# Performance work log

Measured on AMD Instinct MI355X. Metric: run time of the kernel, lower is better.

## Reference

```python
import jax, jax.numpy as jnp
import numpy as np
from jax import lax

B, H_IN, W_IN = 2, 64, 64
C_FEAT = 256
HQ, WQ = 256, 256
HIDDEN_DEPTH = 4
IN_DIM = C_FEAT + 4  # q_feat + rel_coord(2) + rel_cell(2)
OUT_DIM = 2
EPS_SHIFT = 1e-6
CLAMP_EPS = 1e-6


def make_coord(h, w):
    # cell-center coords in [-1,1], dim 0 along H, dim 1 along W (LIIF convention)
    hs = (jnp.arange(h, dtype=jnp.float32) + 0.5) * (2.0 / h) - 1.0
    ws = (jnp.arange(w, dtype=jnp.float32) + 0.5) * (2.0 / w) - 1.0
    return jnp.stack(jnp.meshgrid(hs, ws, indexing='ij'), axis=-1)  # [h,w,2]


def setup_inputs() -> dict:
    key = jax.random.key(0)
    ks = jax.random.split(key, 16)
    inp = jax.random.normal(ks[0], (B, 3, H_IN, W_IN), dtype=jnp.float32)
    coord = jnp.broadcast_to(make_coord(HQ, WQ)[None], (B, HQ, WQ, 2)).astype(jnp.float32)
    cell = jnp.broadcast_to(jnp.array([2.0 / HQ, 2.0 / WQ], dtype=jnp.float32)[None], (B, 2))
    # encoder: single 3x3 conv 3 -> C_FEAT
    conv_w = jax.random.normal(ks[1], (C_FEAT, 3, 3, 3), dtype=jnp.float32) * (1.0 / np.sqrt(3 * 9))
    conv_b = jnp.zeros((C_FEAT,), dtype=jnp.float32)
    # imnet MLP: IN_DIM -> C_FEAT (xHIDDEN_DEPTH, ReLU) -> OUT_DIM
    w_in = jax.random.normal(ks[2], (IN_DIM, C_FEAT), dtype=jnp.float32) * (1.0 / np.sqrt(IN_DIM))
    b_in = jnp.zeros((C_FEAT,), dtype=jnp.float32)
    w_hid = jax.random.normal(ks[3], (HIDDEN_DEPTH - 1, C_FEAT, C_FEAT), dtype=jnp.float32) * (1.0 / np.sqrt(C_FEAT))
    b_hid = jnp.zeros((HIDDEN_DEPTH - 1, C_FEAT), dtype=jnp.float32)
    w_out = jax.random.normal(ks[4], (C_FEAT, OUT_DIM), dtype=jnp.float32) * (1.0 / np.sqrt(C_FEAT))
    b_out = jnp.zeros((OUT_DIM,), dtype=jnp.float32)
    return {"inp": inp, "coord": coord, "cell": cell, "conv_w": conv_w, "conv_b": conv_b,
            "w_in": w_in, "b_in": b_in, "w_hid": w_hid, "b_hid": b_hid,
            "w_out": w_out, "b_out": b_out}


def _mlp(x, w_in, b_in, w_hid, b_hid, w_out, b_out):
    h = jax.nn.relu(x @ w_in + b_in)
    for i in range(w_hid.shape[0]):
        h = jax.nn.relu(h @ w_hid[i] + b_hid[i])
    return h @ w_out + b_out


def _forward(inp, coord, cell, conv_w, conv_b, w_in, b_in, w_hid, b_hid, w_out, b_out):
    feat = lax.conv_general_dilated(inp, conv_w, (1, 1), 'SAME') + conv_b[None, :, None, None]
    Hf, Wf = feat.shape[-2], feat.shape[-1]
    rx = 1.0 / Hf  # 2/H/2
    ry = 1.0 / Wf
    gather = jax.vmap(lambda f, i, j: f[:, i, j])  # [C,H,W],[Hq,Wq]x2 -> [C,Hq,Wq]
    preds, areas = [], []
    for vx in (-1, 1):
        for vy in (-1, 1):
            ch = jnp.clip(coord[..., 0] + vx * rx + EPS_SHIFT, -1 + CLAMP_EPS, 1 - CLAMP_EPS)
            cw = jnp.clip(coord[..., 1] + vy * ry + EPS_SHIFT, -1 + CLAMP_EPS, 1 - CLAMP_EPS)
            # nearest-neighbor grid_sample (align_corners=False): idx = floor((g+1)*size/2)
            ih = jnp.clip(jnp.floor((ch + 1.0) * Hf * 0.5).astype(jnp.int32), 0, Hf - 1)
            iw = jnp.clip(jnp.floor((cw + 1.0) * Wf * 0.5).astype(jnp.int32), 0, Wf - 1)
            q_feat = gather(feat, ih, iw)  # [B,C,Hq,Wq]
            # sampled feat_coord equals cell-center coord of the nearest pixel
            q_ch = (2.0 * ih.astype(jnp.float32) + 1.0) / Hf - 1.0
            q_cw = (2.0 * iw.astype(jnp.float32) + 1.0) / Wf - 1.0
            rel_h = (coord[..., 0] - q_ch) * Hf  # [B,Hq,Wq]
            rel_w = (coord[..., 1] - q_cw) * Wf
            rc_h = jnp.broadcast_to((cell[:, 0] * Hf)[:, None, None], rel_h.shape)
            rc_w = jnp.broadcast_to((cell[:, 1] * Wf)[:, None, None], rel_w.shape)
            x = jnp.concatenate([
                jnp.moveaxis(q_feat, 1, -1),  # [B,Hq,Wq,C]
                rel_h[..., None], rel_w[..., None], rc_h[..., None], rc_w[..., None]
            ], axis=-1)
            preds.append(_mlp(x, w_in, b_in, w_hid, b_hid, w_out, b_out))  # [B,Hq,Wq,2]
            areas.append(jnp.abs(rel_h * rel_w) + 1e-9)
    tot_area = areas[0] + areas[1] + areas[2] + areas[3]
    # local-ensemble diagonal swap
    areas[0], areas[3] = areas[3], areas[0]
    areas[1], areas[2] = areas[2], areas[1]
    ret = sum(p * (a / tot_area)[..., None] for p, a in zip(preds, areas))
    ret = jax.nn.softmax(ret, axis=-1)
    return jnp.moveaxis(ret, -1, 1)  # [B,2,Hq,Wq]


def reference(inp, coord, cell, conv_w, conv_b, w_in, b_in, w_hid, b_hid, w_out, b_out):
    return _forward(inp, coord, cell, conv_w, conv_b, w_in, b_in, w_hid, b_hid, w_out, b_out)
```

## Files before the change

### kernel.cpp

```cpp
#include <hip/hip_runtime.h>

typedef unsigned short ushort_t;
typedef __attribute__((ext_vector_type(8))) _Float16 f16x8;
typedef __attribute__((ext_vector_type(4))) float f32x4;
typedef __attribute__((ext_vector_type(4))) unsigned int u32x4;
typedef __attribute__((ext_vector_type(2))) unsigned long long u64x2;

#define ROWB 576
#define BUFB (64*ROWB)

__device__ __forceinline__ ushort_t f2h(float x){ _Float16 h=(_Float16)x; return __builtin_bit_cast(ushort_t,h); }
__device__ __forceinline__ float h2f(ushort_t u){ return (float)__builtin_bit_cast(_Float16,u); }
__device__ __forceinline__ unsigned int pkrtz(float lo, float hi){
    return __builtin_bit_cast(unsigned int, __builtin_amdgcn_cvt_pkrtz(lo, hi));
}
__device__ __forceinline__ unsigned int pk_add2(unsigned int a, unsigned int b){
    unsigned int r; asm("v_pk_add_f16 %0, %1, %2" : "=v"(r) : "v"(a), "v"(b)); return r;
}
__device__ __forceinline__ unsigned int pk_relu2(unsigned int a){
    unsigned int r; asm("v_pk_max_f16 %0, %1, %2" : "=v"(r) : "v"(a), "v"(0u)); return r;
}

__device__ __forceinline__ int permc(int c){
    return (c & ~31) + (((c >> 2) & 3) << 3) + (c & 3) + (((c >> 4) & 1) << 2);
}

__global__ __launch_bounds__(256) void conv_k(const float* __restrict__ inp,
        const float* __restrict__ w, const float* __restrict__ bias,
        ushort_t* __restrict__ feat)
{
    __shared__ float sw_[6912];
    __shared__ float patch[27];
    int t = threadIdx.x;
    int b = blockIdx.x >> 12, p = blockIdx.x & 4095;
    int y = p >> 6, x = p & 63;
    for (int i = t; i < 6912; i += 256) sw_[i] = w[i];
    if (t < 27){
        int ci = t/9, r = t%9, dy = r/3, dx = r%3;
        int yy = y+dy-1, xx = x+dx-1;
        patch[t] = (yy>=0 && yy<64 && xx>=0 && xx<64) ? inp[((b*3+ci)<<12)+(yy<<6)+xx] : 0.f;
    }
    __syncthreads();
    float acc = bias[t];
    #pragma unroll
    for (int j = 0; j < 27; ++j) acc += patch[j]*sw_[t*27+j];
    feat[(((b<<12)+p)<<8) + permc(t)] = f2h(acc);
}

__global__ __launch_bounds__(256) void pack_k(const float* __restrict__ w_in,
        const float* __restrict__ w_hid, ushort_t* __restrict__ packW)
{
    int i = blockIdx.x*256 + threadIdx.x;
    if (i >= 270336) return;
    int layer, rem;
    if (i < 73728){ layer = 0; rem = i; }
    else { int j = i - 73728; layer = 1 + (j >> 16); rem = j & 65535; }
    int j8 = rem & 7, frag = rem >> 3;
    int lane = frag & 63, kt = frag >> 6;
    int kc = kt >> 4, nt = kt & 15;
    int k = kc*32 + ((lane>>4)<<2) + (j8 & 3) + ((j8 >> 2) << 4);
    int n = (nt<<4) + (lane & 15);
    float val;
    if (layer == 0) val = (k < 260) ? w_in[k*256 + n] : 0.f;
    else            val = w_hid[((layer-1)*256 + k)*256 + n];
    packW[i] = f2h(val);
}

__global__ __launch_bounds__(256) void l0pre_k(const ushort_t* feat,
        const ushort_t* __restrict__ packW, ushort_t* h0)
{
    __shared__ __align__(16) char buf[BUFB];
    const int t = threadIdx.x, lane = t & 63, wave = t >> 6;
    const int b = blockIdx.x >> 6, p0 = (blockIdx.x & 63) << 6;
    {
        int m = t >> 2, q = t & 3;
        char* drow = buf + m*ROWB;
        int sw = ((m & 7) << 4) ^ (q << 4);
        const u64x2* src = (const u64x2*)(feat + (((b<<12) + p0 + m)<<8) + q*64);
        #pragma unroll
        for (int c = 0; c < 8; ++c)
            *(u64x2*)(drow + ((q*128 + c*16) ^ sw)) = src[c];
    }
    __syncthreads();
    const int l15 = lane & 15, g = lane >> 4;
    const int swz = (l15 & 7) << 4;
    f32x4 acc[4][4];
    #pragma unroll
    for (int nt = 0; nt < 4; ++nt)
        #pragma unroll
        for (int mg = 0; mg < 4; ++mg) acc[mg][nt] = (f32x4){0.f,0.f,0.f,0.f};
    const int lofs = (wave*256 + lane)*8;
    f16x8 wA[4], wB[4], aP0[4], aP1[4];
    #pragma unroll
    for (int nt = 0; nt < 4; ++nt){
        wA[nt] = *(const f16x8*)(packW + lofs + nt*512);
        wB[nt] = *(const f16x8*)(packW + lofs + 8192 + nt*512);
    }
    {
        const int o2 = (g*16) ^ swz;
        #pragma unroll
        for (int mg = 0; mg < 4; ++mg)
            aP0[mg] = *(const f16x8*)(buf + (mg*16 + l15)*ROWB + o2);
    }
    #pragma unroll
    for (int kc = 0; kc < 8; ++kc){
        if (kc + 1 < 8){
            const int o2 = ((kc + 1)*64 + g*16) ^ swz ^ ((((kc + 1) >> 1) & 3) << 4);
            if ((kc & 1) == 0){
                #pragma unroll
                for (int mg = 0; mg < 4; ++mg)
                    aP1[mg] = *(const f16x8*)(buf + (mg*16 + l15)*ROWB + o2);
            } else {
                #pragma unroll
                for (int mg = 0; mg < 4; ++mg)
                    aP0[mg] = *(const f16x8*)(buf + (mg*16 + l15)*ROWB + o2);
            }
        }
        if ((kc & 1) == 0){
            #pragma unroll
            for (int mg = 0; mg < 4; ++mg)
                #pragma unroll
                for (int nt = 0; nt < 4; ++nt)
                    acc[mg][nt] = __builtin_amdgcn_mfma_f32_16x16x32_f16(wA[nt], aP0[mg], acc[mg][nt], 0, 0, 0);
        } else {
            #pragma unroll
            for (int mg = 0; mg < 4; ++mg)
                #pragma unroll
                for (int nt = 0; nt < 4; ++nt)
                    acc[mg][nt] = __builtin_amdgcn_mfma_f32_16x16x32_f16(wB[nt], aP1[mg], acc[mg][nt], 0, 0, 0);
        }
        if (kc + 2 < 8){
            const ushort_t* pf = packW + lofs + (kc + 2)*8192;
            if ((kc & 1) == 0){
                #pragma unroll
                for (int nt = 0; nt < 4; ++nt) wA[nt] = *(const f16x8*)(pf + nt*512);
            } else {
                #pragma unroll
                for (int nt = 0; nt < 4; ++nt) wB[nt] = *(const f16x8*)(pf + nt*512);
            }
        }
    }
    #pragma unroll
    for (int mg = 0; mg < 4; ++mg){
        char* row = (char*)(h0 + (((b<<12) + p0 + mg*16 + l15)<<8));
        #pragma unroll
        for (int i = 0; i < 2; ++i){
            const int kb = 2*wave + i;
            f32x4 a0 = acc[mg][2*i], a1 = acc[mg][2*i + 1];
            u32x4 st;
            st[0] = pkrtz(a0[0], a0[1]);
            st[1] = pkrtz(a0[2], a0[3]);
            st[2] = pkrtz(a1[0], a1[1]);
            st[3] = pkrtz(a1[2], a1[3]);
            *(u32x4*)(row + kb*64 + 16*g) = st;
        }
    }
}

template<int KC, bool HAS_NEXT, bool STORE>
__device__ __forceinline__ void mlp_layer(const ushort_t* __restrict__ wfrag,
        const ushort_t* __restrict__ nextw,
        const float* __restrict__ bias, char* __restrict__ buf,
        int lane, int wave, f16x8 (&wP0)[4], f16x8 (&wP1)[4], f32x4 (&acc)[4][4])
{
    const int l15 = lane & 15, g = lane >> 4;
    const int swz  = (l15 & 7) << 4;
    const int aoffg = g*16;
    #pragma unroll
    for (int nt = 0; nt < 4; ++nt){
        f32x4 bv = *(const f32x4*)(bias + (wave*4 + nt)*16 + 4*g);
        #pragma unroll
        for (int mg = 0; mg < 4; ++mg) acc[mg][nt] = bv;
    }
    const int lofs = (wave*4*64 + lane)*8;
    f16x8 aP0[4], aP1[4];
    {
        const int o2 = aoffg ^ swz;
        #pragma unroll
        for (int mg = 0; mg < 4; ++mg)
            aP0[mg] = *(const f16x8*)(buf + (mg*16 + l15)*ROWB + o2);
    }
    #pragma unroll
    for (int kc = 0; kc < KC; ++kc){
        const ushort_t* pfw = nullptr;
        if (kc + 2 < KC)   pfw = wfrag + lofs + (kc + 2)*8192;
        else if (HAS_NEXT) pfw = nextw + lofs + (kc + 2 - KC)*8192;
        const bool la = (kc + 1 < KC);
        if (la){
            const int o2 = ((kc + 1)*64 + aoffg) ^ swz ^ ((((kc + 1) >> 1) & 3) << 4);
            if ((kc & 1) == 0){
                #pragma unroll
                for (int mg = 0; mg < 4; ++mg)
                    aP1[mg] = *(const f16x8*)(buf + (mg*16 + l15)*ROWB + o2);
            } else {
                #pragma unroll
                for (int mg = 0; mg < 4; ++mg)
                    aP0[mg] = *(const f16x8*)(buf + (mg*16 + l15)*ROWB + o2);
            }
        }
        __builtin_amdgcn_s_setprio(1);
        if ((kc & 1) == 0){
            #pragma unroll
            for (int mg = 0; mg < 4; ++mg)
                #pragma unroll
                for (int nt = 0; nt < 4; ++nt)
                    acc[mg][nt] = __builtin_amdgcn_mfma_f32_16x16x32_f16(wP0[nt], aP0[mg], acc[mg][nt], 0, 0, 0);
        } else {
            #pragma unroll
            for (int mg = 0; mg < 4; ++mg)
                #pragma unroll
                for (int nt = 0; nt < 4; ++nt)
                    acc[mg][nt] = __builtin_amdgcn_mfma_f32_16x16x32_f16(wP1[nt], aP1[mg], acc[mg][nt], 0, 0, 0);
        }
        __builtin_amdgcn_s_setprio(0);
        if (pfw){
            if ((kc & 1) == 0){
                #pragma unroll
                for (int nt = 0; nt < 4; ++nt) wP0[nt] = *(const f16x8*)(pfw + nt*512);
            } else {
                #pragma unroll
                for (int nt = 0; nt < 4; ++nt) wP1[nt] = *(const f16x8*)(pfw + nt*512);
            }
        }
    }
    __syncthreads();
    if (STORE){
        const int wsw = swz ^ (wave << 4);
        #pragma unroll
        for (int mg = 0; mg < 4; ++mg){
            char* row = buf + (mg*16 + l15)*ROWB;
            #pragma unroll
            for (int i = 0; i < 2; ++i){
                const int kb = 2*wave + i;
                f32x4 a0 = acc[mg][2*i], a1 = acc[mg][2*i + 1];
                u32x4 st;
                st[0] = pk_relu2(pkrtz(a0[0], a0[1]));
                st[1] = pk_relu2(pkrtz(a0[2], a0[3]));
                st[2] = pk_relu2(pkrtz(a1[0], a1[1]));
                st[3] = pk_relu2(pkrtz(a1[2], a1[3]));
                *(u32x4*)(row + ((kb*64 + 16*g) ^ wsw)) = st;
            }
        }
        __syncthreads();
    }
}

__global__ __launch_bounds__(256, 3) void liif_k(
        const float* __restrict__ coord, const float* __restrict__ cell,
        const float* __restrict__ b_in, const float* __restrict__ b_hid,
        const float* __restrict__ w_out, const float* __restrict__ b_out,
        const ushort_t* __restrict__ h0, const ushort_t* __restrict__ packW,
        float* __restrict__ out)
{
    __shared__ __align__(16) char buf[BUFB];
    __shared__ float sarea[64];
    const int t = threadIdx.x, lane = t & 63, wave = t >> 6;
    const int bi = blockIdx.x;
    const int b = bi >> 12;
    const int t12 = bi & 4095;
    const int th = t12 >> 6, tw = t12 & 63;

    f16x8 wX[4], wA[4], wB[4];
    const ushort_t* L1 = packW + 73728;
    {
        const int lofs = (wave*256 + lane)*8;
        #pragma unroll
        for (int nt = 0; nt < 4; ++nt){
            wX[nt] = *(const f16x8*)(packW + 65536 + lofs + nt*512);
            wA[nt] = *(const f16x8*)(L1 + lofs + nt*512);
            wB[nt] = *(const f16x8*)(L1 + 8192 + nt*512 + lofs);
        }
    }

    {
        int m = t >> 2, q = t & 3;
        int v = m >> 4, pix = m & 15;
        int qh = th*4 + (pix >> 2), qw = tw*4 + (pix & 3);
        int cidx = (((b<<8) + qh)<<8) + qw;
        float c0 = coord[cidx*2], c1 = coord[cidx*2 + 1];
        float ch = c0 + ((v & 2) ? 0.015625f : -0.015625f); ch = ch + 1e-6f;
        ch = fminf(fmaxf(ch, -1.f + 1e-6f), 1.f - 1e-6f);
        float cw = c1 + ((v & 1) ? 0.015625f : -0.015625f); cw = cw + 1e-6f;
        cw = fminf(fmaxf(cw, -1.f + 1e-6f), 1.f - 1e-6f);
        int ih = (int)floorf((ch + 1.f)*64.f*0.5f); ih = ih < 0 ? 0 : (ih > 63 ? 63 : ih);
        int iw = (int)floorf((cw + 1.f)*64.f*0.5f); iw = iw < 0 ? 0 : (iw > 63 ? 63 : iw);
        char* drow = buf + m*ROWB;
        int sw = ((m & 7) << 4) ^ (q << 4);
        const u64x2* src = (const u64x2*)(h0 + ((((b<<6) + ih)<<6) + iw)*256 + q*64);
        #pragma unroll
        for (int c = 0; c < 8; ++c)
            *(u64x2*)(drow + ((q*128 + c*16) ^ sw)) = src[c];
        if (q == 0){
            float qch = (2.f*(float)ih + 1.f)*(1.f/64.f) - 1.f;
            float qcw = (2.f*(float)iw + 1.f)*(1.f/64.f) - 1.f;
            float relh = (c0 - qch)*64.f, relw = (c1 - qcw)*64.f;
            float rch = cell[b*2]*64.f, rcw = cell[b*2 + 1]*64.f;
            unsigned long long ex = (unsigned long long)f2h(relh)
                | ((unsigned long long)f2h(relw) << 16)
                | ((unsigned long long)f2h(rch)  << 32)
                | ((unsigned long long)f2h(rcw)  << 48);
            u64x2 e; e[0] = ex; e[1] = 0;
            u64x2 z; z[0] = 0;  z[1] = 0;
            int sw2 = (m & 3) << 4;
            #pragma unroll
            for (int c = 1; c < 4; ++c)
                *(u64x2*)(drow + 512 + ((c*16) ^ sw2)) = z;
            *(u64x2*)(drow + 512 + sw2) = e;
            sarea[m] = fabsf(relh*relw) + 1e-9f;
        }
    }
    __syncthreads();

    f32x4 acc[4][4];
    {
        const int l15 = lane & 15, g = lane >> 4;
        const int swz  = (l15 & 7) << 4;
        const int swz2 = (l15 & 3) << 4;
        const int wsw  = swz ^ (wave << 4);
        #pragma unroll
        for (int nt = 0; nt < 4; ++nt){
            f32x4 bv = *(const f32x4*)(b_in + (wave*4 + nt)*16 + 4*g);
            #pragma unroll
            for (int mg = 0; mg < 4; ++mg) acc[mg][nt] = bv;
        }
        f16x8 af[4];
        {
            const int o2 = 512 + ((g*16) ^ swz2);
            #pragma unroll
            for (int mg = 0; mg < 4; ++mg)
                af[mg] = *(const f16x8*)(buf + (mg*16 + l15)*ROWB + o2);
        }
        #pragma unroll
        for (int mg = 0; mg < 4; ++mg)
            #pragma unroll
            for (int nt = 0; nt < 4; ++nt)
                acc[mg][nt] = __builtin_amdgcn_mfma_f32_16x16x32_f16(wX[nt], af[mg], acc[mg][nt], 0, 0, 0);
        #pragma unroll
        for (int mg = 0; mg < 4; ++mg){
            char* row = buf + (mg*16 + l15)*ROWB;
            #pragma unroll
            for (int i = 0; i < 2; ++i){
                const int kb = 2*wave + i;
                u32x4 hv = *(const u32x4*)(row + ((kb*64 + 16*g) ^ wsw));
                f32x4 a0 = acc[mg][2*i], a1 = acc[mg][2*i + 1];
                u32x4 st;
                st[0] = pk_relu2(pk_add2(pkrtz(a0[0], a0[1]), hv[0]));
                st[1] = pk_relu2(pk_add2(pkrtz(a0[2], a0[3]), hv[1]));
                st[2] = pk_relu2(pk_add2(pkrtz(a1[0], a1[1]), hv[2]));
                st[3] = pk_relu2(pk_add2(pkrtz(a1[2], a1[3]), hv[3]));
                *(u32x4*)(row + ((kb*64 + 16*g) ^ wsw)) = st;
            }
        }
        __syncthreads();
    }

    const ushort_t* L2 = packW + 73728 + 65536;
    const ushort_t* L3 = packW + 73728 + 131072;
    mlp_layer<8, true , true >(L1, L2,      b_hid,       buf, lane, wave, wA, wB, acc);
    mlp_layer<8, true , true >(L2, L3,      b_hid + 256, buf, lane, wave, wA, wB, acc);
    mlp_layer<8, false, false>(L3, nullptr, b_hid + 512, buf, lane, wave, wA, wB, acc);

    {
        const int l15 = lane & 15, g = lane >> 4;
        float s0[4] = {0.f,0.f,0.f,0.f}, s1[4] = {0.f,0.f,0.f,0.f};
        #pragma unroll
        for (int j = 0; j < 4; ++j){
            int nb = wave*64 + j*16 + 4*g;
            f32x4 w01 = *(const f32x4*)(w_out + nb*2);
            f32x4 w23 = *(const f32x4*)(w_out + nb*2 + 4);
            #pragma unroll
            for (int mg = 0; mg < 4; ++mg){
                float v0 = fmaxf(acc[mg][j][0], 0.f);
                float v1 = fmaxf(acc[mg][j][1], 0.f);
                float v2 = fmaxf(acc[mg][j][2], 0.f);
                float v3 = fmaxf(acc[mg][j][3], 0.f);
                s0[mg] += v0*w01[0] + v1*w01[2] + v2*w23[0] + v3*w23[2];
                s1[mg] += v0*w01[1] + v1*w01[3] + v2*w23[1] + v3*w23[3];
            }
        }
        float2* stage  = (float2*)buf;
        float2* stage2 = (float2*)(buf + 2048);
        #pragma unroll
        for (int mg = 0; mg < 4; ++mg){
            s0[mg] += __shfl_xor(s0[mg], 16); s0[mg] += __shfl_xor(s0[mg], 32);
            s1[mg] += __shfl_xor(s1[mg], 16); s1[mg] += __shfl_xor(s1[mg], 32);
            if (lane < 16){
                float2 pr; pr.x = s0[mg]; pr.y = s1[mg];
                stage[wave*64 + mg*16 + l15] = pr;
            }
        }
        __syncthreads();
        if (t < 64){
            float2 p0 = stage[t], p1 = stage[64 + t], p2 = stage[128 + t], p3 = stage[192 + t];
            float2 pr;
            pr.x = p0.x + p1.x + p2.x + p3.x;
            pr.y = p0.y + p1.y + p2.y + p3.y;
            stage2[t] = pr;
        }
        __syncthreads();
        if (t < 16){
            float2 pv[4]; float a[4];
            #pragma unroll
            for (int v = 0; v < 4; ++v){
                pv[v] = stage2[v*16 + t];
                a[v]  = sarea[v*16 + t];
            }
            float tot = a[0] + a[1] + a[2] + a[3];
            float w0 = a[3]/tot, w1 = a[2]/tot, w2 = a[1]/tot, w3 = a[0]/tot;
            float r0 = pv[0].x*w0 + pv[1].x*w1 + pv[2].x*w2 + pv[3].x*w3 + b_out[0];
            float r1 = pv[0].y*w0 + pv[1].y*w1 + pv[2].y*w2 + pv[3].y*w3 + b_out[1];
            float mx = fmaxf(r0, r1);
            float e0 = expf(r0 - mx), e1 = expf(r1 - mx);
            float inv = 1.f/(e0 + e1);
            int qh = th*4 + (t >> 2), qw = tw*4 + (t & 3);
            int qidx = (qh << 8) + qw;
            out[(b<<17) + qidx]         = e0*inv;
            out[(b<<17) + 65536 + qidx] = e1*inv;
        }
    }
}

extern "C" void kernel_launch(void* const* d_in, const int* in_sizes, int n_in,
                              void* d_out, int out_size, void* d_ws, size_t ws_size,
                              hipStream_t stream)
{
    const float* inp   = (const float*)d_in[0];
    const float* coord = (const float*)d_in[1];
    const float* cell  = (const float*)d_in[2];
    const float* convw = (const float*)d_in[3];
    const float* convb = (const float*)d_in[4];
    const float* w_in  = (const float*)d_in[5];
    const float* b_in  = (const float*)d_in[6];
    const float* w_hid = (const float*)d_in[7];
    const float* b_hid = (const float*)d_in[8];
    const float* w_out = (const float*)d_in[9];
    const float* b_out = (const float*)d_in[10];
    (void)in_sizes; (void)n_in; (void)out_size; (void)ws_size;

    char* ws = (char*)d_ws;
    ushort_t* feat  = (ushort_t*)ws;
    ushort_t* packW = (ushort_t*)(ws + 4194304);
    float* out = (float*)d_out;

    pack_k<<<dim3(1056), dim3(256), 0, stream>>>(w_in, w_hid, packW);
    conv_k<<<dim3(8192), dim3(256), 0, stream>>>(inp, convw, convb, feat);
    l0pre_k<<<dim3(128), dim3(256), 0, stream>>>(feat, packW, feat);
    liif_k<<<dim3(8192), dim3(256), 0, stream>>>(coord, cell, b_in, b_hid,
                                                 w_out, b_out, feat, packW, out);
}
```

Measured before the change: 258.1 us.

## Fuse 3x3 conv into layer-0 pre-GEMM kernel using MFMA on 8x8 spatial tiles

Removes the separate per-pixel scalar conv kernel, which ran 8192 blocks each reloading the full conv weights. The conv is now computed inside the layer-0 projection kernel as a K=32 MFMA over im2col patches built in LDS from 8x8 spatial tiles. The fp16 result goes back into LDS, so the full feature map no longer makes a round trip through global memory. Conv weights are packed to fp16 fragments alongside the MLP weights. This adds fp16 rounding of conv inputs and weights, and rows of h0 are now written in tile order.

```diff
diff --git a/kernel.cpp b/kernel.cpp
--- a/kernel.cpp
+++ b/kernel.cpp
@@ -25,33 +25,21 @@
     return (c & ~31) + (((c >> 2) & 3) << 3) + (c & 3) + (((c >> 4) & 1) << 2);
 }
 
-__global__ __launch_bounds__(256) void conv_k(const float* __restrict__ inp,
-        const float* __restrict__ w, const float* __restrict__ bias,
-        ushort_t* __restrict__ feat)
-{
-    __shared__ float sw_[6912];
-    __shared__ float patch[27];
-    int t = threadIdx.x;
-    int b = blockIdx.x >> 12, p = blockIdx.x & 4095;
-    int y = p >> 6, x = p & 63;
-    for (int i = t; i < 6912; i += 256) sw_[i] = w[i];
-    if (t < 27){
-        int ci = t/9, r = t%9, dy = r/3, dx = r%3;
-        int yy = y+dy-1, xx = x+dx-1;
-        patch[t] = (yy>=0 && yy<64 && xx>=0 && xx<64) ? inp[((b*3+ci)<<12)+(yy<<6)+xx] : 0.f;
-    }
-    __syncthreads();
-    float acc = bias[t];
-    #pragma unroll
-    for (int j = 0; j < 27; ++j) acc += patch[j]*sw_[t*27+j];
-    feat[(((b<<12)+p)<<8) + permc(t)] = f2h(acc);
-}
-
 __global__ __launch_bounds__(256) void pack_k(const float* __restrict__ w_in,
-        const float* __restrict__ w_hid, ushort_t* __restrict__ packW)
+        const float* __restrict__ w_hid, const float* __restrict__ convw,
+        ushort_t* __restrict__ packW)
 {
     int i = blockIdx.x*256 + threadIdx.x;
-    if (i >= 270336) return;
+    if (i >= 278528) return;
+    if (i >= 270336){
+        int j = i - 270336;
+        int j8 = j & 7, frag = j >> 3;
+        int lane = frag & 63, nt = frag >> 6;
+        int k = ((lane>>4)<<2) + (j8 & 3) + ((j8 >> 2) << 4);
+        int n = (nt<<4) + (lane & 15);
+        packW[i] = f2h(k < 27 ? convw[n*27 + k] : 0.f);
+        return;
+    }
     int layer, rem;
     if (i < 73728){ layer = 0; rem = i; }
     else { int j = i - 73728; layer = 1 + (j >> 16); rem = j & 65535; }
@@ -66,83 +54,156 @@
     packW[i] = f2h(val);
 }
 
-__global__ __launch_bounds__(256) void l0pre_k(const ushort_t* feat,
-        const ushort_t* __restrict__ packW, ushort_t* h0)
+__global__ __launch_bounds__(256) void convl0_k(const float* __restrict__ inp,
+        const float* __restrict__ convb, const ushort_t* __restrict__ packW,
+        ushort_t* __restrict__ h0)
 {
     __shared__ __align__(16) char buf[BUFB];
+    __shared__ float patch[300];
     const int t = threadIdx.x, lane = t & 63, wave = t >> 6;
-    const int b = blockIdx.x >> 6, p0 = (blockIdx.x & 63) << 6;
+    const int b = blockIdx.x >> 6, tile = blockIdx.x & 63;
+    const int ty = tile >> 3, tx = tile & 7;
+
+    for (int i = t; i < 300; i += 256){
+        int ci = i / 100, rem = i % 100, py = rem / 10, px = rem % 10;
+        int gy = ty*8 + py - 1, gx = tx*8 + px - 1;
+        patch[i] = (gy >= 0 && gy < 64 && gx >= 0 && gx < 64)
+                 ? inp[((b*3 + ci) << 12) + (gy << 6) + gx] : 0.f;
+    }
+    __syncthreads();
+
     {
         int m = t >> 2, q = t & 3;
-        char* drow = buf + m*ROWB;
-        int sw = ((m & 7) << 4) ^ (q << 4);
-        const u64x2* src = (const u64x2*)(feat + (((b<<12) + p0 + m)<<8) + q*64);
-        #pragma unroll
-        for (int c = 0; c < 8; ++c)
-            *(u64x2*)(drow + ((q*128 + c*16) ^ sw)) = src[c];
+        int my = m >> 3, mx = m & 7;
+        ushort_t vals[8];
+        #pragma unroll
+        for (int j = 0; j < 8; ++j){
+            int k = 4*q + (j & 3) + ((j >> 2) << 4);
+            float v = 0.f;
+            if (k < 27){
+                int ci = k / 9, r = k % 9;
+                v = patch[ci*100 + (my + r/3)*10 + (mx + r%3)];
+            }
+            vals[j] = f2h(v);
+        }
+        u64x2 st;
+        st[0] = (unsigned long long)vals[0] | ((unsigned long long)vals[1] << 16)
+              | ((unsigned long long)vals[2] << 32) | ((unsigned long long)vals[3] << 48);
+        st[1] = (unsigned long long)vals[4] | ((unsigned long long)vals[5] << 16)
+              | ((unsigned long long)vals[6] << 32) | ((unsigned long long)vals[7] << 48);
+        *(u64x2*)(buf + m*ROWB + ((q*16) ^ ((m & 7) << 4))) = st;
     }
     __syncthreads();
+
     const int l15 = lane & 15, g = lane >> 4;
     const int swz = (l15 & 7) << 4;
     f32x4 acc[4][4];
+
+    #pragma unroll
+    for (int nt = 0; nt < 4; ++nt){
+        f32x4 bv = *(const f32x4*)(convb + (wave*4 + nt)*16 + 4*g);
+        #pragma unroll
+        for (int mg = 0; mg < 4; ++mg) acc[mg][nt] = bv;
+    }
+    {
+        const ushort_t* packC = packW + 270336;
+        const int lofs = (wave*4*64 + lane)*8;
+        f16x8 wc[4], af[4];
+        #pragma unroll
+        for (int nt = 0; nt < 4; ++nt) wc[nt] = *(const f16x8*)(packC + lofs + nt*512);
+        #pragma unroll
+        for (int mg = 0; mg < 4; ++mg)
+            af[mg] = *(const f16x8*)(buf + (mg*16 + l15)*ROWB + ((g*16) ^ swz));
+        #pragma unroll
+        for (int mg = 0; mg < 4; ++mg)
+            #pragma unroll
+            for (int nt = 0; nt < 4; ++nt)
+                acc[mg][nt] = __builtin_amdgcn_mfma_f32_16x16x32_f16(wc[nt], af[mg], acc[mg][nt], 0, 0, 0);
+    }
+    __syncthreads();
+
+    {
+        const int wsw = swz ^ (wave << 4);
+        #pragma unroll
+        for (int mg = 0; mg < 4; ++mg){
+            char* row = buf + (mg*16 + l15)*ROWB;
+            #pragma unroll
+            for (int i = 0; i < 2; ++i){
+                const int kb = 2*wave + i;
+                f32x4 a0 = acc[mg][2*i], a1 = acc[mg][2*i + 1];
+                u32x4 st;
+                st[0] = pkrtz(a0[0], a0[1]);
+                st[1] = pkrtz(a0[2], a0[3]);
+                st[2] = pkrtz(a1[0], a1[1]);
+                st[3] = pkrtz(a1[2], a1[3]);
+                *(u32x4*)(row + ((kb*64 + 16*g) ^ wsw)) = st;
+            }
+        }
+    }
+    __syncthreads();
+
     #pragma unroll
     for (int nt = 0; nt < 4; ++nt)
         #pragma unroll
         for (int mg = 0; mg < 4; ++mg) acc[mg][nt] = (f32x4){0.f,0.f,0.f,0.f};
-    const int lofs = (wave*256 + lane)*8;
-    f16x8 wA[4], wB[4], aP0[4], aP1[4];
-    #pragma unroll
-    for (int nt = 0; nt < 4; ++nt){
-        wA[nt] = *(const f16x8*)(packW + lofs + nt*512);
-        wB[nt] = *(const f16x8*)(packW + lofs + 8192 + nt*512);
-    }
-    {
-        const int o2 = (g*16) ^ swz;
-        #pragma unroll
-        for (int mg = 0; mg < 4; ++mg)
-            aP0[mg] = *(const f16x8*)(buf + (mg*16 + l15)*ROWB + o2);
-    }
-    #pragma unroll
-    for (int kc = 0; kc < 8; ++kc){
-        if (kc + 1 < 8){
-            const int o2 = ((kc + 1)*64 + g*16) ^ swz ^ ((((kc + 1) >> 1) & 3) << 4);
+    {
+        const int lofs = (wave*256 + lane)*8;
+        f16x8 wA[4], wB[4], aP0[4], aP1[4];
+        #pragma unroll
+        for (int nt = 0; nt < 4; ++nt){
+            wA[nt] = *(const f16x8*)(packW + lofs + nt*512);
+            wB[nt] = *(const f16x8*)(packW + lofs + 8192 + nt*512);
+        }
+        {
+            const int o2 = (g*16) ^ swz;
+            #pragma unroll
+            for (int mg = 0; mg < 4; ++mg)
+                aP0[mg] = *(const f16x8*)(buf + (mg*16 + l15)*ROWB + o2);
+        }
+        #pragma unroll
+        for (int kc = 0; kc < 8; ++kc){
+            if (kc + 1 < 8){
+                const int o2 = ((kc + 1)*64 + g*16) ^ swz ^ ((((kc + 1) >> 1) & 3) << 4);
+                if ((kc & 1) == 0){
+                    #pragma unroll
+                    for (int mg = 0; mg < 4; ++mg)
+                        aP1[mg] = *(const f16x8*)(buf + (mg*16 + l15)*ROWB + o2);
+                } else {
+                    #pragma unroll
+                    for (int mg = 0; mg < 4; ++mg)
+                        aP0[mg] = *(const f16x8*)(buf + (mg*16 + l15)*ROWB + o2);
+                }
+            }
             if ((kc & 1) == 0){
                 #pragma unroll
                 for (int mg = 0; mg < 4; ++mg)
-                    aP1[mg] = *(const f16x8*)(buf + (mg*16 + l15)*ROWB + o2);
+                    #pragma unroll
+                    for (int nt = 0; nt < 4; ++nt)
+                        acc[mg][nt] = __builtin_amdgcn_mfma_f32_16x16x32_f16(wA[nt], aP0[mg], acc[mg][nt], 0, 0, 0);
             } else {
                 #pragma unroll
                 for (int mg = 0; mg < 4; ++mg)
-                    aP0[mg] = *(const f16x8*)(buf + (mg*16 + l15)*ROWB + o2);
-            }
-        }
-        if ((kc & 1) == 0){
-            #pragma unroll
-            for (int mg = 0; mg < 4; ++mg)
-                #pragma unroll
-                for (int nt = 0; nt < 4; ++nt)
-                    acc[mg][nt] = __builtin_amdgcn_mfma_f32_16x16x32_f16(wA[nt], aP0[mg], acc[mg][nt], 0, 0, 0);
-        } else {
-            #pragma unroll
-            for (int mg = 0; mg < 4; ++mg)
-                #pragma unroll
-                for (int nt = 0; nt < 4; ++nt)
-                    acc[mg][nt] = __builtin_amdgcn_mfma_f32_16x16x32_f16(wB[nt], aP1[mg], acc[mg][nt], 0, 0, 0);
-        }
-        if (kc + 2 < 8){
-            const ushort_t* pf = packW + lofs + (kc + 2)*8192;
-            if ((kc & 1) == 0){
-                #pragma unroll
-                for (int nt = 0; nt < 4; ++nt) wA[nt] = *(const f16x8*)(pf + nt*512);
-            } else {
-                #pragma unroll
-                for (int nt = 0; nt < 4; ++nt) wB[nt] = *(const f16x8*)(pf + nt*512);
+                    #pragma unroll
+                    for (int nt = 0; nt < 4; ++nt)
+                        acc[mg][nt] = __builtin_amdgcn_mfma_f32_16x16x32_f16(wB[nt], aP1[mg], acc[mg][nt], 0, 0, 0);
+            }
+            if (kc + 2 < 8){
+                const ushort_t* pf = packW + lofs + (kc + 2)*8192;
+                if ((kc & 1) == 0){
+                    #pragma unroll
+                    for (int nt = 0; nt < 4; ++nt) wA[nt] = *(const f16x8*)(pf + nt*512);
+                } else {
+                    #pragma unroll
+                    for (int nt = 0; nt < 4; ++nt) wB[nt] = *(const f16x8*)(pf + nt*512);
+                }
             }
         }
     }
     #pragma unroll
     for (int mg = 0; mg < 4; ++mg){
-        char* row = (char*)(h0 + (((b<<12) + p0 + mg*16 + l15)<<8));
+        const int m = mg*16 + l15;
+        const int p = ((ty*8 + (m >> 3)) << 6) + tx*8 + (m & 7);
+        char* row = (char*)(h0 + (((b<<12) + p)<<8));
         #pragma unroll
         for (int i = 0; i < 2; ++i){
             const int kb = 2*wave + i;
@@ -438,13 +499,12 @@
     (void)in_sizes; (void)n_in; (void)out_size; (void)ws_size;
 
     char* ws = (char*)d_ws;
-    ushort_t* feat  = (ushort_t*)ws;
+    ushort_t* h0    = (ushort_t*)ws;
     ushort_t* packW = (ushort_t*)(ws + 4194304);
     float* out = (float*)d_out;
 
-    pack_k<<<dim3(1056), dim3(256), 0, stream>>>(w_in, w_hid, packW);
-    conv_k<<<dim3(8192), dim3(256), 0, stream>>>(inp, convw, convb, feat);
-    l0pre_k<<<dim3(128), dim3(256), 0, stream>>>(feat, packW, feat);
+    pack_k<<<dim3(1088), dim3(256), 0, stream>>>(w_in, w_hid, convw, packW);
+    convl0_k<<<dim3(128), dim3(256), 0, stream>>>(inp, convb, packW, h0);
     liif_k<<<dim3(8192), dim3(256), 0, stream>>>(coord, cell, b_in, b_hid,
-                                                 w_out, b_out, feat, packW, out);
-}
+                                                 w_out, b_out, h0, packW, out);
+}
```

Measured after the change: 239.4 us. 1.08x faster.
